# Optimization experiments

Hardware: AMD Instinct MI355X
Metric: run time of the kernel (lower is better)

## Reference

```python
import jax, jax.numpy as jnp
import numpy as np

N_NODES = 100000
N_EDGES = 1600000
N_GRAPHS = 2048
HID = 64
IN_F = 14
N_CLS = 2
EPS = 1e-5


def _gcn_conv(x, row, col, w_edge, W, b, n_nodes):
    # PyG GCNConv with add_self_loops=True, normalize=True.
    xw = x @ W  # [N, out]
    # degree on target nodes, self-loop contributes weight 1
    deg = jnp.zeros((n_nodes,), x.dtype).at[col].add(w_edge) + 1.0
    dinv = deg ** -0.5
    norm = dinv[row] * w_edge * dinv[col]  # [E]
    out = jnp.zeros_like(xw).at[col].add(norm[:, None] * xw[row])
    out = out + (dinv * dinv)[:, None] * xw  # self-loop term
    return out + b


def _bn_relu(x, gamma, beta):
    mean = jnp.mean(x, axis=0)
    var = jnp.var(x, axis=0)  # biased, as PyTorch BN training normalization
    y = gamma * (x - mean) * jax.lax.rsqrt(var + EPS) + beta
    return jax.nn.relu(y)


def setup_inputs() -> dict:
    key = jax.random.key(0)
    ks = jax.random.split(key, 8)
    x = jax.random.normal(ks[0], (N_NODES, IN_F), dtype=jnp.float32)
    edge_index = jax.random.randint(ks[1], (2, N_EDGES), 0, N_NODES, dtype=jnp.int64)
    batch = jnp.sort(jax.random.randint(ks[2], (N_NODES,), 0, N_GRAPHS, dtype=jnp.int64))
    edge_weight = jnp.ones((N_EDGES,), dtype=jnp.float32)
    def lin(k, fi, fo):
        s = 1.0 / np.sqrt(fi)
        kw, kb = jax.random.split(k)
        return (jax.random.uniform(kw, (fi, fo), jnp.float32, -s, s),
                jax.random.uniform(kb, (fo,), jnp.float32, -s, s))
    W1, b1 = lin(ks[3], IN_F, HID)
    W2, b2 = lin(ks[4], HID, HID)
    W3, b3 = lin(ks[5], HID, HID)
    fcW, fcb = lin(ks[6], HID, N_CLS)
    g = jnp.ones((HID,), jnp.float32)
    z = jnp.zeros((HID,), jnp.float32)
    return {
        "x": x, "edge_index": edge_index, "batch": batch, "edge_weight": edge_weight,
        "W1": W1, "b1": b1, "W2": W2, "b2": b2, "W3": W3, "b3": b3,
        "g1": g, "bt1": z, "g2": g, "bt2": z, "g3": g, "bt3": z,
        "fcW": fcW, "fcb": fcb,
    }


def reference(x, edge_index, batch, edge_weight, W1, b1, W2, b2, W3, b3,
              g1, bt1, g2, bt2, g3, bt3, fcW, fcb):
    row, col = edge_index[0], edge_index[1]
    n = x.shape[0]
    h = _bn_relu(_gcn_conv(x, row, col, edge_weight, W1, b1, n), g1, bt1)
    h = _bn_relu(_gcn_conv(h, row, col, edge_weight, W2, b2, n), g2, bt2)
    h = _bn_relu(_gcn_conv(h, row, col, edge_weight, W3, b3, n), g3, bt3)
    node_embs = h  # dropout p=0 is identity
    graph_emb = jax.ops.segment_sum(node_embs, batch, num_segments=N_GRAPHS)
    out = graph_emb @ fcW + fcb
    return (out, node_embs, graph_emb)
```

## Files before the change

### kernel.cpp

```cpp
#include <hip/hip_runtime.h>
#include <hip/hip_fp16.h>

#define N_NODES 100000
#define N_EDGES 1600000
#define EMAX2   2000000
#define N_GRAPHS 2048
#define HID 64
#define IN_F 14
#define N_CLS 2
#define EPS 1e-5f

#define BSHIFT 9
#define NBUCK 196
#define ABLOCKS 256
#define CHUNK (N_EDGES / ABLOCKS)

#define NBLK2 128
#define NCHUNK2 ((N_NODES + NBLK2 - 1) / NBLK2)

typedef _Float16 half_t;
typedef _Float16 half8 __attribute__((ext_vector_type(8)));
typedef float f32x4 __attribute__((ext_vector_type(4)));

#define GSTRIDE ((size_t)N_NODES * 16)


__global__ __launch_bounds__(256) void histA_kernel(const int* __restrict__ col,
                                                    int* __restrict__ histG) {
    __shared__ int hl[NBUCK];
    for (int i = threadIdx.x; i < NBUCK; i += 256) hl[i] = 0;
    __syncthreads();
    int e0 = blockIdx.x * CHUNK;
    for (int e = e0 + threadIdx.x; e < e0 + CHUNK; e += 256)
        atomicAdd(&hl[col[e] >> BSHIFT], 1);
    __syncthreads();
    for (int i = threadIdx.x; i < NBUCK; i += 256)
        histG[i * ABLOCKS + blockIdx.x] = hl[i];
}

__global__ __launch_bounds__(256) void scanS1_kernel(const int* __restrict__ histG,
                                                     int* __restrict__ bsumA) {
    __shared__ int ls[256];
    ls[threadIdx.x] = histG[blockIdx.x * 256 + threadIdx.x];
    __syncthreads();
    for (int off = 128; off > 0; off >>= 1) {
        if (threadIdx.x < off) ls[threadIdx.x] += ls[threadIdx.x + off];
        __syncthreads();
    }
    if (threadIdx.x == 0) bsumA[blockIdx.x] = ls[0];
}

__global__ __launch_bounds__(512) void topscan_kernel(int* __restrict__ bsum, int nb) {
    __shared__ int ls[512];
    int t = threadIdx.x;
    int v = (t < nb) ? bsum[t] : 0;
    ls[t] = v;
    __syncthreads();
    for (int off = 1; off < 512; off <<= 1) {
        int x = ls[t];
        if (t >= off) x += ls[t - off];
        __syncthreads();
        ls[t] = x;
        __syncthreads();
    }
    if (t < nb) bsum[t] = ls[t] - v;
}

__global__ __launch_bounds__(256) void scanS3_kernel(int* __restrict__ histG,
                                                     const int* __restrict__ bsumA,
                                                     int* __restrict__ ptr) {
    __shared__ int ls[256];
    int idx = blockIdx.x * 256 + threadIdx.x;
    int v = histG[idx];
    ls[threadIdx.x] = v;
    __syncthreads();
    for (int off = 1; off < 256; off <<= 1) {
        int x = ls[threadIdx.x];
        if (threadIdx.x >= off) x += ls[threadIdx.x - off];
        __syncthreads();
        ls[threadIdx.x] = x;
        __syncthreads();
    }
    histG[idx] = ls[threadIdx.x] - v + bsumA[blockIdx.x];
    if (blockIdx.x == 0 && threadIdx.x == 0) ptr[N_NODES] = N_EDGES;
}

__global__ __launch_bounds__(256) void scatterA_kernel(const int* __restrict__ row,
                                                       const int* __restrict__ col,
                                                       const float* __restrict__ w,
                                                       const int* __restrict__ histG,
                                                       int2* __restrict__ EA) {
    __shared__ int cur[NBUCK];
    for (int i = threadIdx.x; i < NBUCK; i += 256)
        cur[i] = histG[i * ABLOCKS + blockIdx.x];
    __syncthreads();
    int e0 = blockIdx.x * CHUNK;
    for (int e = e0 + threadIdx.x; e < e0 + CHUNK; e += 256) {
        int c = col[e];
        int r = row[e];
        int fx = (int)__float2uint_rn(w[e] * 8192.0f);
        int pos = atomicAdd(&cur[c >> BSHIFT], 1);
        EA[pos] = make_int2(r, (fx << 17) | c);
    }
}

__global__ __launch_bounds__(256) void bucketA_kernel(const int2* __restrict__ EA,
                                                      const int* __restrict__ bsumA,
                                                      int* __restrict__ ptr,
                                                      float* __restrict__ dinv) {
    __shared__ int hist[512], wsum[512];
    int b = blockIdx.x;
    int beg = bsumA[b];
    int end = (b == NBUCK - 1) ? N_EDGES : bsumA[b + 1];
    int i0 = threadIdx.x, i1 = threadIdx.x + 256;
    hist[i0] = 0; hist[i1] = 0;
    wsum[i0] = 0; wsum[i1] = 0;
    __syncthreads();
    for (int e = beg + threadIdx.x; e < end; e += 256) {
        int2 ed = EA[e];
        int c9 = ed.y & 511;
        atomicAdd(&hist[c9], 1);
        atomicAdd(&wsum[c9], (int)((unsigned int)ed.y >> 17));
    }
    __syncthreads();
    int cnt0 = hist[i0], cnt1 = hist[i1];
    for (int off = 1; off < 512; off <<= 1) {
        int v0 = hist[i0], v1 = hist[i1];
        int a0 = (i0 >= off) ? hist[i0 - off] : 0;
        int a1 = (i1 >= off) ? hist[i1 - off] : 0;
        __syncthreads();
        hist[i0] = v0 + a0;
        hist[i1] = v1 + a1;
        __syncthreads();
    }
    int excl0 = hist[i0] - cnt0, excl1 = hist[i1] - cnt1;
    int col0 = (b << BSHIFT) + i0, col1 = (b << BSHIFT) + i1;
    if (col0 < N_NODES) {
        ptr[col0] = beg + excl0;
        dinv[col0] = rsqrtf(1.0f + (float)wsum[i0] * (1.0f / 8192.0f));
    }
    if (col1 < N_NODES) {
        ptr[col1] = beg + excl1;
        dinv[col1] = rsqrtf(1.0f + (float)wsum[i1] * (1.0f / 8192.0f));
    }
}


__global__ __launch_bounds__(256) void histD_kernel(const int* __restrict__ ptr,
                                                    int* __restrict__ histD) {
    __shared__ int hl[2048];
    for (int i = threadIdx.x; i < 2048; i += 256) hl[i] = 0;
    __syncthreads();
    int n0 = blockIdx.x * NCHUNK2;
    int n1 = n0 + NCHUNK2; if (n1 > N_NODES) n1 = N_NODES;
    for (int n = n0 + threadIdx.x; n < n1; n += 256) {
        int d = ptr[n + 1] - ptr[n];
        if (d > 255) d = 255;
        atomicAdd(&hl[((threadIdx.x & 7) << 8) + d], 1);
    }
    __syncthreads();
    int s = 0;
#pragma unroll
    for (int c = 0; c < 8; c++) s += hl[(c << 8) + threadIdx.x];
    histD[threadIdx.x * NBLK2 + blockIdx.x] = s;
}

__global__ __launch_bounds__(128) void scanD1_kernel(const int* __restrict__ histD,
                                                     int* __restrict__ rowTot) {
    __shared__ int ls[128];
    ls[threadIdx.x] = histD[blockIdx.x * NBLK2 + threadIdx.x];
    __syncthreads();
    for (int off = 64; off > 0; off >>= 1) {
        if (threadIdx.x < off) ls[threadIdx.x] += ls[threadIdx.x + off];
        __syncthreads();
    }
    if (threadIdx.x == 0) rowTot[blockIdx.x] = ls[0];
}

__global__ __launch_bounds__(256) void topscanD_kernel(const int* __restrict__ rowTot,
                                                       int* __restrict__ nodeExcl,
                                                       int* __restrict__ edgeExcl,
                                                       int* __restrict__ ptrS) {
    __shared__ int a[256], b[256];
    int t = threadIdx.x;
    int cnt = rowTot[t];
    int dpad = (t + 3) & ~3;
    int ec = cnt * dpad;
    a[t] = cnt; b[t] = ec;
    __syncthreads();
    for (int off = 1; off < 256; off <<= 1) {
        int va = a[t], vb = b[t];
        if (t >= off) { va += a[t - off]; vb += b[t - off]; }
        __syncthreads();
        a[t] = va; b[t] = vb;
        __syncthreads();
    }
    nodeExcl[t] = a[t] - cnt;
    edgeExcl[t] = b[t] - ec;
    if (t == 255) ptrS[N_NODES] = b[255];
}

__global__ __launch_bounds__(128) void scanD3_kernel(int* __restrict__ histD,
                                                     const int* __restrict__ nodeExcl) {
    __shared__ int ls[128];
    int idx = blockIdx.x * NBLK2 + threadIdx.x;
    int v = histD[idx];
    ls[threadIdx.x] = v;
    __syncthreads();
    for (int off = 1; off < 128; off <<= 1) {
        int x = ls[threadIdx.x];
        if (threadIdx.x >= off) x += ls[threadIdx.x - off];
        __syncthreads();
        ls[threadIdx.x] = x;
        __syncthreads();
    }
    histD[idx] = ls[threadIdx.x] - v + nodeExcl[blockIdx.x];
}

__global__ __launch_bounds__(256) void scatterD_kernel(const int* __restrict__ ptr,
                                                       const int* __restrict__ histD,
                                                       const int* __restrict__ nodeExcl,
                                                       const int* __restrict__ edgeExcl,
                                                       int* __restrict__ perm,
                                                       int* __restrict__ ptrS,
                                                       int* __restrict__ newbase) {
    __shared__ int cur[256];
    cur[threadIdx.x] = histD[threadIdx.x * NBLK2 + blockIdx.x];
    __syncthreads();
    int n0 = blockIdx.x * NCHUNK2;
    int n1 = n0 + NCHUNK2; if (n1 > N_NODES) n1 = N_NODES;
    for (int n = n0 + threadIdx.x; n < n1; n += 256) {
        int d = ptr[n + 1] - ptr[n];
        if (d > 255) d = 255;
        int dpad = (d + 3) & ~3;
        int pos = atomicAdd(&cur[d], 1);
        int ebase = edgeExcl[d] + (pos - nodeExcl[d]) * dpad;
        perm[pos] = n;
        ptrS[pos] = ebase;
        newbase[n] = ebase;
    }
}

__global__ __launch_bounds__(256) void bucketB_kernel(const int2* __restrict__ EA,
                                                      const int* __restrict__ bsumA,
                                                      const int* __restrict__ newbase,
                                                      const float* __restrict__ dinv,
                                                      unsigned int* __restrict__ srcoff,
                                                      half_t* __restrict__ normh) {
    __shared__ int cur[512];
    int b = blockIdx.x;
    int beg = bsumA[b];
    int end = (b == NBUCK - 1) ? N_EDGES : bsumA[b + 1];
    int i0 = threadIdx.x, i1 = threadIdx.x + 256;
    int col0 = (b << BSHIFT) + i0, col1 = (b << BSHIFT) + i1;
    cur[i0] = (col0 < N_NODES) ? newbase[col0] : 0;
    cur[i1] = (col1 < N_NODES) ? newbase[col1] : 0;
    __syncthreads();
    for (int e = beg + threadIdx.x; e < end; e += 256) {
        int2 ed = EA[e];
        int c = ed.y & 0x1ffff;
        float w = (float)((unsigned int)ed.y >> 17) * (1.0f / 8192.0f);
        float nrm = dinv[ed.x] * w * dinv[c];
        int pos = atomicAdd(&cur[c & 511], 1);
        srcoff[pos] = (unsigned int)ed.x << 5;
        normh[pos] = (half_t)nrm;
    }
}


template <int K>
__global__ __launch_bounds__(256) void gemm_kernel(const float* __restrict__ h,
                                                   const float* __restrict__ W,
                                                   half_t* __restrict__ xw, int n_nodes) {
    int f = threadIdx.x & 63;
    float wcol[K];
#pragma unroll
    for (int k = 0; k < K; k++) wcol[k] = W[k * HID + f];
    half_t* xg = xw + (size_t)(f >> 4) * GSTRIDE + (f & 15);
    int wave = (blockIdx.x * blockDim.x + threadIdx.x) >> 6;
    int nwaves = (gridDim.x * blockDim.x) >> 6;
    for (int n = wave; n < n_nodes; n += nwaves) {
        const float* hr = h + (size_t)n * K;
        float acc = 0.f;
#pragma unroll
        for (int k = 0; k < K; k++) acc += hr[k] * wcol[k];
        xg[(size_t)n * 16] = (half_t)acc;
    }
}

__global__ __launch_bounds__(256) void gemm_bn_mfma_kernel(const half_t* __restrict__ h,
                                                           const float* __restrict__ W,
                                                           const float* __restrict__ stats,
                                                           const float* __restrict__ gamma,
                                                           const float* __restrict__ beta,
                                                           half_t* __restrict__ xw, int n_nodes) {
    __shared__ float sc_s[HID], sh_s[HID];
    if (threadIdx.x < 64) {
        float mean = stats[threadIdx.x] * (1.0f / N_NODES);
        float var = stats[64 + threadIdx.x] * (1.0f / N_NODES) - mean * mean;
        float sc = gamma[threadIdx.x] * rsqrtf(var + EPS);
        sc_s[threadIdx.x] = sc;
        sh_s[threadIdx.x] = beta[threadIdx.x] - mean * sc;
    }
    __syncthreads();
    int lane = threadIdx.x & 63;
    int col16 = lane & 15;
    int quad = lane >> 4;

    float scA[2][8], shA[2][8];
#pragma unroll
    for (int kh = 0; kh < 2; kh++)
#pragma unroll
        for (int j = 0; j < 8; j++) {
            int k = kh * 32 + quad * 8 + j;
            scA[kh][j] = sc_s[k];
            shA[kh][j] = sh_s[k];
        }

    half8 bfrag[4][2];
#pragma unroll
    for (int t = 0; t < 4; t++)
#pragma unroll
        for (int kh = 0; kh < 2; kh++)
#pragma unroll
            for (int j = 0; j < 8; j++) {
                int k = kh * 32 + quad * 8 + j;
                bfrag[t][kh][j] = (half_t)W[k * HID + t * 16 + col16];
            }

    int wave = (blockIdx.x * blockDim.x + threadIdx.x) >> 6;
    int nwaves = (gridDim.x * blockDim.x) >> 6;
    int ntiles = n_nodes >> 4;
    for (int tIdx = wave; tIdx < ntiles; tIdx += nwaves) {
        int n0 = tIdx << 4;
        half8 afrag[2];
#pragma unroll
        for (int kh = 0; kh < 2; kh++) {
            int k0 = kh * 32 + quad * 8;
            const half_t* hp = h + (size_t)(k0 >> 4) * GSTRIDE
                                 + (size_t)(n0 + col16) * 16 + (k0 & 15);
            half8 raw = *(const half8*)hp;
#pragma unroll
            for (int j = 0; j < 8; j++) {
                float v = (float)raw[j] * scA[kh][j] + shA[kh][j];
                afrag[kh][j] = (half_t)fmaxf(v, 0.f);
            }
        }
        f32x4 acc[4];
#pragma unroll
        for (int t = 0; t < 4; t++) {
            f32x4 z = {0.f, 0.f, 0.f, 0.f};
            acc[t] = __builtin_amdgcn_mfma_f32_16x16x32_f16(afrag[0], bfrag[t][0], z, 0, 0, 0);
            acc[t] = __builtin_amdgcn_mfma_f32_16x16x32_f16(afrag[1], bfrag[t][1], acc[t], 0, 0, 0);
        }
#pragma unroll
        for (int t = 0; t < 4; t++) {
            half_t* xg = xw + (size_t)t * GSTRIDE;
#pragma unroll
            for (int r = 0; r < 4; r++) {
                int rowi = n0 + quad * 4 + r;
                xg[(size_t)rowi * 16 + col16] = (half_t)acc[t][r];
            }
        }
    }
}

__global__ __launch_bounds__(256) void gather_stats_kernel(const int* __restrict__ ptrS,
                                                           const int* __restrict__ perm,
                                                           const unsigned int* __restrict__ srcoff,
                                                           const unsigned int* __restrict__ normu,
                                                           const half_t* __restrict__ xw,
                                                           const float* __restrict__ dinv,
                                                           const float* __restrict__ b,
                                                           half_t* __restrict__ hp,
                                                           float* __restrict__ stats,
                                                           int n_nodes) {
    int g = (blockIdx.x & 7) >> 1;
    int grank = ((blockIdx.x >> 3) << 1) | (blockIdx.x & 1);
    int lane16 = threadIdx.x & 15;
    int quadLocal = threadIdx.x >> 4;
    int quadId = grank * 16 + quadLocal;
    int nquads = (gridDim.x >> 2) * 16;

    const half_t* xg = xw + (size_t)g * GSTRIDE;
    const char* xgc = (const char*)xg;
    unsigned int loff = (unsigned int)(lane16 * 2);
    half_t* hpg = hp + (size_t)g * GSTRIDE;
    int f = g * 16 + lane16;
    float bf = b[f];
    int base = ((threadIdx.x & 63) >> 4) * 16;

    float s = 0.f, s2 = 0.f;

    int npairs = n_nodes >> 1;
    int idx = quadId;
    int nodeA = 0, begA = 0, cA = 0, nodeB = 0, begB = 0, cB = 0;
    int evA = 0, nvA = 0, evB = 0, nvB = 0;
    if (idx < npairs) {
        int iA = idx * 2;
        nodeA = perm[iA];
        nodeB = perm[iA + 1];
        begA = ptrS[iA];
        begB = ptrS[iA + 1];
        cA = begB - begA;
        cB = ptrS[iA + 2] - begB;
        int mA = (cA > 16) ? 16 : cA;
        int mB = (cB > 16) ? 16 : cB;
        if (lane16 < mA) evA = (int)srcoff[begA + lane16];
        if (lane16 < (mA >> 1)) nvA = (int)normu[(begA >> 1) + lane16];
        if (lane16 < mB) evB = (int)srcoff[begB + lane16];
        if (lane16 < (mB >> 1)) nvB = (int)normu[(begB >> 1) + lane16];
    }

    while (idx < npairs) {
        int inext = idx + nquads;
        int nodeA2 = 0, begA2 = 0, cA2 = 0, nodeB2 = 0, begB2 = 0, cB2 = 0;
        if (inext < npairs) {
            int iN = inext * 2;
            nodeA2 = perm[iN];
            nodeB2 = perm[iN + 1];
            begA2 = ptrS[iN];
            begB2 = ptrS[iN + 1];
            cA2 = begB2 - begA2;
            cB2 = ptrS[iN + 2] - begB2;
        }
        float selfA = (float)xg[(size_t)nodeA * 16 + lane16];
        float diA = dinv[nodeA];
        float selfB = (float)xg[(size_t)nodeB * 16 + lane16];
        float diB = dinv[nodeB];

        __half2 aA0 = __float2half2_rn(0.f), aA1 = __float2half2_rn(0.f);
        __half2 aB0 = __float2half2_rn(0.f), aB1 = __float2half2_rn(0.f);

        for (int j0 = 0; j0 < cB; j0 += 16) {
            int mA = cA - j0; mA = (mA < 0) ? 0 : ((mA > 16) ? 16 : mA);
            int mB = cB - j0; mB = (mB > 16) ? 16 : mB;
            int pA = mA >> 1;
            int pB = mB >> 1;
            int evA2 = 0, nvA2 = 0, evB2 = 0, nvB2 = 0;
            int j1 = j0 + 16;
            if (j1 < cA) {
                int m2 = cA - j1; if (m2 > 16) m2 = 16;
                if (lane16 < m2) evA2 = (int)srcoff[begA + j1 + lane16];
                if (lane16 < (m2 >> 1)) nvA2 = (int)normu[((begA + j1) >> 1) + lane16];
            }
            if (j1 < cB) {
                int m2 = cB - j1; if (m2 > 16) m2 = 16;
                if (lane16 < m2) evB2 = (int)srcoff[begB + j1 + lane16];
                if (lane16 < (m2 >> 1)) nvB2 = (int)normu[((begB + j1) >> 1) + lane16];
            }
            for (int p = 0; p < pB; p += 2) {
                unsigned int ub0 = (unsigned int)__shfl(evB, base + 2 * p);
                unsigned int ub1 = (unsigned int)__shfl(evB, base + 2 * p + 1);
                unsigned int ub2 = (unsigned int)__shfl(evB, base + 2 * p + 2);
                unsigned int ub3 = (unsigned int)__shfl(evB, base + 2 * p + 3);
                unsigned int nb0 = (unsigned int)__shfl(nvB, base + p);
                unsigned int nb1 = (unsigned int)__shfl(nvB, base + p + 1);
                __half hb0 = *(const __half*)(xgc + (ub0 + loff));
                __half hb1 = *(const __half*)(xgc + (ub1 + loff));
                __half hb2 = *(const __half*)(xgc + (ub2 + loff));
                __half hb3 = *(const __half*)(xgc + (ub3 + loff));
                aB0 = __hfma2(*(__half2*)&nb0, __halves2half2(hb0, hb1), aB0);
                aB1 = __hfma2(*(__half2*)&nb1, __halves2half2(hb2, hb3), aB1);
                if (p < pA) {
                    unsigned int ua0 = (unsigned int)__shfl(evA, base + 2 * p);
                    unsigned int ua1 = (unsigned int)__shfl(evA, base + 2 * p + 1);
                    unsigned int ua2 = (unsigned int)__shfl(evA, base + 2 * p + 2);
                    unsigned int ua3 = (unsigned int)__shfl(evA, base + 2 * p + 3);
                    unsigned int na0 = (unsigned int)__shfl(nvA, base + p);
                    unsigned int na1 = (unsigned int)__shfl(nvA, base + p + 1);
                    __half ha0 = *(const __half*)(xgc + (ua0 + loff));
                    __half ha1 = *(const __half*)(xgc + (ua1 + loff));
                    __half ha2 = *(const __half*)(xgc + (ua2 + loff));
                    __half ha3 = *(const __half*)(xgc + (ua3 + loff));
                    aA0 = __hfma2(*(__half2*)&na0, __halves2half2(ha0, ha1), aA0);
                    aA1 = __hfma2(*(__half2*)&na1, __halves2half2(ha2, ha3), aA1);
                }
            }
            evA = evA2; nvA = nvA2; evB = evB2; nvB = nvB2;
        }
        if (inext < npairs) {
            int mA0 = (cA2 > 16) ? 16 : cA2;
            int mB0 = (cB2 > 16) ? 16 : cB2;
            evA = (lane16 < mA0) ? (int)srcoff[begA2 + lane16] : 0;
            nvA = (lane16 < (mA0 >> 1)) ? (int)normu[(begA2 >> 1) + lane16] : 0;
            evB = (lane16 < mB0) ? (int)srcoff[begB2 + lane16] : 0;
            nvB = (lane16 < (mB0 >> 1)) ? (int)normu[(begB2 >> 1) + lane16] : 0;
        }

        float accA = (__low2float(aA0) + __high2float(aA0))
                   + (__low2float(aA1) + __high2float(aA1));
        float vA = accA + diA * diA * selfA + bf;
        hpg[(size_t)nodeA * 16 + lane16] = (half_t)vA;
        float accB = (__low2float(aB0) + __high2float(aB0))
                   + (__low2float(aB1) + __high2float(aB1));
        float vB = accB + diB * diB * selfB + bf;
        hpg[(size_t)nodeB * 16 + lane16] = (half_t)vB;
        s += vA + vB;
        s2 += vA * vA + vB * vB;

        idx = inext;
        nodeA = nodeA2; begA = begA2; cA = cA2;
        nodeB = nodeB2; begB = begB2; cB = cB2;
    }
    __shared__ float ls[256], ls2[256];
    ls[threadIdx.x] = s;
    ls2[threadIdx.x] = s2;
    __syncthreads();
    if (threadIdx.x < 16) {
        float a = 0.f, aa = 0.f;
#pragma unroll
        for (int k = 0; k < 16; k++) {
            a += ls[k * 16 + threadIdx.x];
            aa += ls2[k * 16 + threadIdx.x];
        }
        atomicAdd(&stats[g * 16 + threadIdx.x], a);
        atomicAdd(&stats[64 + g * 16 + threadIdx.x], aa);
    }
}

__global__ __launch_bounds__(256) void bn_relu_seg_kernel(const half_t* __restrict__ hpl,
                                                          float* __restrict__ h3,
                                                          const float* __restrict__ stats,
                                                          const float* __restrict__ gamma,
                                                          const float* __restrict__ beta,
                                                          const int* __restrict__ batch,
                                                          float* __restrict__ gemb,
                                                          int n_nodes) {
    int g = blockIdx.x * blockDim.x + threadIdx.x;
    int f = g & 63;
    int wave = g >> 6;
    int nwaves = (gridDim.x * blockDim.x) >> 6;
    int chunk = (n_nodes + nwaves - 1) / nwaves;
    int n0 = wave * chunk;
    int n1 = n0 + chunk;
    if (n1 > n_nodes) n1 = n_nodes;
    if (n0 >= n_nodes) return;
    float mean = stats[f] * (1.0f / N_NODES);
    float var = stats[64 + f] * (1.0f / N_NODES) - mean * mean;
    float sc = gamma[f] * rsqrtf(var + EPS);
    float sh = beta[f] - mean * sc;
    const half_t* hg = hpl + (size_t)(f >> 4) * GSTRIDE + (f & 15);
    int curg = batch[n0];
    float racc = 0.f;
    for (int n = n0; n < n1; n++) {
        int bg = batch[n];
        if (bg != curg) {
            atomicAdd(&gemb[(size_t)curg * HID + f], racc);
            racc = 0.f;
            curg = bg;
        }
        float v = (float)hg[(size_t)n * 16] * sc + sh;
        v = fmaxf(v, 0.f);
        h3[(size_t)n * HID + f] = v;
        racc += v;
    }
    atomicAdd(&gemb[(size_t)curg * HID + f], racc);
}

__global__ __launch_bounds__(256) void final_kernel(const float* __restrict__ gemb,
                                                    const float* __restrict__ fcW,
                                                    const float* __restrict__ fcb,
                                                    float* __restrict__ out) {
    int g = blockIdx.x * blockDim.x + threadIdx.x;
    if (g >= N_GRAPHS * N_CLS) return;
    int gr = g >> 1, c = g & 1;
    float acc = fcb[c];
#pragma unroll
    for (int k = 0; k < HID; k++) acc += gemb[gr * HID + k] * fcW[k * N_CLS + c];
    out[g] = acc;
}


extern "C" void kernel_launch(void* const* d_in, const int* in_sizes, int n_in,
                              void* d_out, int out_size, void* d_ws, size_t ws_size,
                              hipStream_t stream) {
    const float* x    = (const float*)d_in[0];
    const int*   ei   = (const int*)d_in[1];
    const int*   batch= (const int*)d_in[2];
    const float* ew   = (const float*)d_in[3];
    const float* W1   = (const float*)d_in[4];
    const float* b1   = (const float*)d_in[5];
    const float* W2   = (const float*)d_in[6];
    const float* b2   = (const float*)d_in[7];
    const float* W3   = (const float*)d_in[8];
    const float* b3   = (const float*)d_in[9];
    const float* g1   = (const float*)d_in[10];
    const float* bt1  = (const float*)d_in[11];
    const float* g2   = (const float*)d_in[12];
    const float* bt2  = (const float*)d_in[13];
    const float* g3   = (const float*)d_in[14];
    const float* bt3  = (const float*)d_in[15];
    const float* fcW  = (const float*)d_in[16];
    const float* fcb  = (const float*)d_in[17];

    const int* row = ei;
    const int* col = ei + N_EDGES;

    float* out_head  = (float*)d_out;
    float* node_embs = out_head + N_GRAPHS * N_CLS;
    float* gemb      = node_embs + (size_t)N_NODES * HID;

    char* bse = (char*)d_ws;
    half_t* xwh = (half_t*)bse;
    char* r1 = bse + (size_t)N_NODES * HID * 2;
    int2*   EA  = (int2*)r1;
    half_t* hpl = (half_t*)r1;
    char* r2 = r1 + (size_t)N_NODES * HID * 2;
    unsigned int* srcoff = (unsigned int*)r2;
    half_t* normh = (half_t*)(srcoff + EMAX2);
    char* r3 = r2 + (size_t)EMAX2 * 6;
    float* dinv  = (float*)r3;
    float* stats3 = dinv + N_NODES;
    int*   ptr   = (int*)(stats3 + 384);
    int*   histG = ptr + N_NODES + 1;
    int*   bsumA = histG + NBUCK * ABLOCKS;
    int*   histD = bsumA + NBUCK + 4;
    int*   rowTot = histD + 256 * NBLK2;
    int*   nodeExcl = rowTot + 256;
    int*   edgeExcl = nodeExcl + 256;
    int*   perm   = edgeExcl + 256;
    int*   newbase= perm + N_NODES;
    int*   ptrS   = newbase + N_NODES;

    const int B   = 256;
    const int gGS = 1024;
    const int gGA = 2048;

    hipMemsetAsync(srcoff, 0, (size_t)EMAX2 * 6, stream);
    hipMemsetAsync(stats3, 0, 384 * sizeof(float), stream);
    hipMemsetAsync(gemb, 0, (size_t)N_GRAPHS * HID * sizeof(float), stream);

    histA_kernel<<<ABLOCKS, B, 0, stream>>>(col, histG);
    scanS1_kernel<<<NBUCK, B, 0, stream>>>(histG, bsumA);
    topscan_kernel<<<1, 512, 0, stream>>>(bsumA, NBUCK);
    scanS3_kernel<<<NBUCK, B, 0, stream>>>(histG, bsumA, ptr);
    scatterA_kernel<<<ABLOCKS, B, 0, stream>>>(row, col, ew, histG, EA);
    bucketA_kernel<<<NBUCK, B, 0, stream>>>(EA, bsumA, ptr, dinv);

    histD_kernel<<<NBLK2, B, 0, stream>>>(ptr, histD);
    scanD1_kernel<<<256, 128, 0, stream>>>(histD, rowTot);
    topscanD_kernel<<<1, 256, 0, stream>>>(rowTot, nodeExcl, edgeExcl, ptrS);
    scanD3_kernel<<<256, 128, 0, stream>>>(histD, nodeExcl);
    scatterD_kernel<<<NBLK2, B, 0, stream>>>(ptr, histD, nodeExcl, edgeExcl,
                                             perm, ptrS, newbase);
    bucketB_kernel<<<NBUCK, B, 0, stream>>>(EA, bsumA, newbase, dinv, srcoff, normh);

    float* h3 = node_embs;

    gemm_kernel<IN_F><<<gGS, B, 0, stream>>>(x, W1, xwh, N_NODES);
    gather_stats_kernel<<<gGA, B, 0, stream>>>(ptrS, perm, srcoff,
                                               (const unsigned int*)normh, xwh,
                                               dinv, b1, hpl, stats3, N_NODES);

    gemm_bn_mfma_kernel<<<gGS, B, 0, stream>>>(hpl, W2, stats3, g1, bt1, xwh, N_NODES);
    gather_stats_kernel<<<gGA, B, 0, stream>>>(ptrS, perm, srcoff,
                                               (const unsigned int*)normh, xwh,
                                               dinv, b2, hpl, stats3 + 128, N_NODES);

    gemm_bn_mfma_kernel<<<gGS, B, 0, stream>>>(hpl, W3, stats3 + 128, g2, bt2, xwh, N_NODES);
    gather_stats_kernel<<<gGA, B, 0, stream>>>(ptrS, perm, srcoff,
                                               (const unsigned int*)normh, xwh,
                                               dinv, b3, hpl, stats3 + 256, N_NODES);

    bn_relu_seg_kernel<<<gGS, B, 0, stream>>>(hpl, h3, stats3 + 256, g3, bt3,
                                              batch, gemb, N_NODES);

    final_kernel<<<(N_GRAPHS * N_CLS + B - 1) / B, B, 0, stream>>>(gemb, fcW, fcb, out_head);
}
```

Before: 414.7 us.

## Fold dinv scaling into GEMM output, balance gather work, fuse scans and memsets

The symmetric normalization is restructured so the GEMM outputs are pre-scaled by dinv[src] and the gather applies dinv[dst] once, which lets the edge stream carry raw weights instead of per-edge norms. A new qbounds kernel binary-searches the padded edge prefix so each quad gets a contiguous, roughly equal-work range of nodes instead of a strided slice. The top-level scan kernels are folded into the per-block scan kernels. The large memsets are replaced by zeroing only the padding slots and by clearing gemb and stats inside histA. This removes several launches and a large memset, and trims per-edge gather loads, at the cost of redundant scan work in every block and reliance on the padding being zeroed so the gather can read full 16-lane groups unconditionally.

```diff
diff --git a/kernel.cpp b/kernel.cpp
--- a/kernel.cpp
+++ b/kernel.cpp
@@ -18,6 +18,8 @@
 #define NBLK2 128
 #define NCHUNK2 ((N_NODES + NBLK2 - 1) / NBLK2)
 
+#define NQUADS 8192
+
 typedef _Float16 half_t;
 typedef _Float16 half8 __attribute__((ext_vector_type(8)));
 typedef float f32x4 __attribute__((ext_vector_type(4)));
@@ -26,9 +28,14 @@
 
 
 __global__ __launch_bounds__(256) void histA_kernel(const int* __restrict__ col,
-                                                    int* __restrict__ histG) {
+                                                    int* __restrict__ histG,
+                                                    float* __restrict__ gemb,
+                                                    float* __restrict__ stats3) {
     __shared__ int hl[NBUCK];
     for (int i = threadIdx.x; i < NBUCK; i += 256) hl[i] = 0;
+    for (int k = threadIdx.x; k < 512; k += 256)
+        gemb[(size_t)blockIdx.x * 512 + k] = 0.f;
+    if (blockIdx.x == 0 && threadIdx.x < 384) stats3[threadIdx.x] = 0.f;
     __syncthreads();
     int e0 = blockIdx.x * CHUNK;
     for (int e = e0 + threadIdx.x; e < e0 + CHUNK; e += 256)
@@ -50,39 +57,30 @@
     if (threadIdx.x == 0) bsumA[blockIdx.x] = ls[0];
 }
 
-__global__ __launch_bounds__(512) void topscan_kernel(int* __restrict__ bsum, int nb) {
-    __shared__ int ls[512];
-    int t = threadIdx.x;
-    int v = (t < nb) ? bsum[t] : 0;
-    ls[t] = v;
-    __syncthreads();
-    for (int off = 1; off < 512; off <<= 1) {
-        int x = ls[t];
-        if (t >= off) x += ls[t - off];
-        __syncthreads();
-        ls[t] = x;
-        __syncthreads();
-    }
-    if (t < nb) bsum[t] = ls[t] - v;
-}
-
 __global__ __launch_bounds__(256) void scanS3_kernel(int* __restrict__ histG,
                                                      const int* __restrict__ bsumA,
+                                                     int* __restrict__ bsumX,
                                                      int* __restrict__ ptr) {
-    __shared__ int ls[256];
-    int idx = blockIdx.x * 256 + threadIdx.x;
+    __shared__ int ls[256], bs[256];
+    int t = threadIdx.x;
+    int rawB = (blockIdx.x < NBUCK) ? bsumA[blockIdx.x] : 0;
+    bs[t] = (t < NBUCK) ? bsumA[t] : 0;
+    int idx = blockIdx.x * 256 + t;
     int v = histG[idx];
-    ls[threadIdx.x] = v;
+    ls[t] = v;
     __syncthreads();
     for (int off = 1; off < 256; off <<= 1) {
-        int x = ls[threadIdx.x];
-        if (threadIdx.x >= off) x += ls[threadIdx.x - off];
-        __syncthreads();
-        ls[threadIdx.x] = x;
-        __syncthreads();
-    }
-    histG[idx] = ls[threadIdx.x] - v + bsumA[blockIdx.x];
-    if (blockIdx.x == 0 && threadIdx.x == 0) ptr[N_NODES] = N_EDGES;
+        int x = ls[t];
+        int y = bs[t];
+        if (t >= off) { x += ls[t - off]; y += bs[t - off]; }
+        __syncthreads();
+        ls[t] = x; bs[t] = y;
+        __syncthreads();
+    }
+    int bexcl = bs[blockIdx.x] - rawB;
+    histG[idx] = ls[t] - v + bexcl;
+    if (t == 0) bsumX[blockIdx.x] = bexcl;
+    if (blockIdx.x == 0 && t == 0) ptr[N_NODES] = N_EDGES;
 }
 
 __global__ __launch_bounds__(256) void scatterA_kernel(const int* __restrict__ row,
@@ -105,13 +103,13 @@
 }
 
 __global__ __launch_bounds__(256) void bucketA_kernel(const int2* __restrict__ EA,
-                                                      const int* __restrict__ bsumA,
+                                                      const int* __restrict__ bsumX,
                                                       int* __restrict__ ptr,
                                                       float* __restrict__ dinv) {
     __shared__ int hist[512], wsum[512];
     int b = blockIdx.x;
-    int beg = bsumA[b];
-    int end = (b == NBUCK - 1) ? N_EDGES : bsumA[b + 1];
+    int beg = bsumX[b];
+    int end = (b == NBUCK - 1) ? N_EDGES : bsumX[b + 1];
     int i0 = threadIdx.x, i1 = threadIdx.x + 256;
     hist[i0] = 0; hist[i1] = 0;
     wsum[i0] = 0; wsum[i1] = 0;
@@ -177,44 +175,50 @@
     if (threadIdx.x == 0) rowTot[blockIdx.x] = ls[0];
 }
 
-__global__ __launch_bounds__(256) void topscanD_kernel(const int* __restrict__ rowTot,
-                                                       int* __restrict__ nodeExcl,
-                                                       int* __restrict__ edgeExcl,
-                                                       int* __restrict__ ptrS) {
-    __shared__ int a[256], b[256];
+__global__ __launch_bounds__(128) void scanD3_kernel(int* __restrict__ histD,
+                                                     const int* __restrict__ rowTot,
+                                                     int* __restrict__ nodeExcl,
+                                                     int* __restrict__ edgeExcl,
+                                                     int* __restrict__ ptrS) {
+    __shared__ int ls[128], sa[256], sb[256];
     int t = threadIdx.x;
-    int cnt = rowTot[t];
-    int dpad = (t + 3) & ~3;
-    int ec = cnt * dpad;
-    a[t] = cnt; b[t] = ec;
+    int bin = blockIdx.x;
+    int c0 = rowTot[t], c1 = rowTot[t + 128];
+    sa[t] = c0;           sa[t + 128] = c1;
+    sb[t] = c0 * ((t + 3) & ~3);
+    sb[t + 128] = c1 * ((t + 131) & ~3);
+    int idx = bin * NBLK2 + t;
+    int v = histD[idx];
+    ls[t] = v;
     __syncthreads();
     for (int off = 1; off < 256; off <<= 1) {
-        int va = a[t], vb = b[t];
-        if (t >= off) { va += a[t - off]; vb += b[t - off]; }
-        __syncthreads();
-        a[t] = va; b[t] = vb;
-        __syncthreads();
-    }
-    nodeExcl[t] = a[t] - cnt;
-    edgeExcl[t] = b[t] - ec;
-    if (t == 255) ptrS[N_NODES] = b[255];
-}
-
-__global__ __launch_bounds__(128) void scanD3_kernel(int* __restrict__ histD,
-                                                     const int* __restrict__ nodeExcl) {
-    __shared__ int ls[128];
-    int idx = blockIdx.x * NBLK2 + threadIdx.x;
-    int v = histD[idx];
-    ls[threadIdx.x] = v;
-    __syncthreads();
+        int a0 = sa[t], a1 = sa[t + 128];
+        int b0 = sb[t], b1 = sb[t + 128];
+        int x0 = (t >= off) ? sa[t - off] : 0;
+        int x1 = (t + 128 >= off) ? sa[t + 128 - off] : 0;
+        int y0 = (t >= off) ? sb[t - off] : 0;
+        int y1 = (t + 128 >= off) ? sb[t + 128 - off] : 0;
+        __syncthreads();
+        sa[t] = a0 + x0; sa[t + 128] = a1 + x1;
+        sb[t] = b0 + y0; sb[t + 128] = b1 + y1;
+        __syncthreads();
+    }
     for (int off = 1; off < 128; off <<= 1) {
-        int x = ls[threadIdx.x];
-        if (threadIdx.x >= off) x += ls[threadIdx.x - off];
-        __syncthreads();
-        ls[threadIdx.x] = x;
-        __syncthreads();
-    }
-    histD[idx] = ls[threadIdx.x] - v + nodeExcl[blockIdx.x];
+        int x = ls[t];
+        if (t >= off) x += ls[t - off];
+        __syncthreads();
+        ls[t] = x;
+        __syncthreads();
+    }
+    int nE = sa[bin] - rowTot[bin];
+    histD[idx] = ls[t] - v + nE;
+    if (bin == 0) {
+        nodeExcl[t] = sa[t] - rowTot[t];
+        nodeExcl[t + 128] = sa[t + 128] - rowTot[t + 128];
+        edgeExcl[t] = sb[t] - rowTot[t] * ((t + 3) & ~3);
+        edgeExcl[t + 128] = sb[t + 128] - rowTot[t + 128] * ((t + 131) & ~3);
+        if (t == 127) ptrS[N_NODES] = sb[255];
+    }
 }
 
 __global__ __launch_bounds__(256) void scatterD_kernel(const int* __restrict__ ptr,
@@ -223,7 +227,9 @@
                                                        const int* __restrict__ edgeExcl,
                                                        int* __restrict__ perm,
                                                        int* __restrict__ ptrS,
-                                                       int* __restrict__ newbase) {
+                                                       int* __restrict__ newbase,
+                                                       unsigned int* __restrict__ srcoff,
+                                                       half_t* __restrict__ normh) {
     __shared__ int cur[256];
     cur[threadIdx.x] = histD[threadIdx.x * NBLK2 + blockIdx.x];
     __syncthreads();
@@ -238,19 +244,38 @@
         perm[pos] = n;
         ptrS[pos] = ebase;
         newbase[n] = ebase;
-    }
+        for (int k = d; k < dpad; k++) {
+            srcoff[ebase + k] = 0u;
+            normh[ebase + k] = (half_t)0.f;
+        }
+    }
+}
+
+__global__ __launch_bounds__(256) void qbounds_kernel(const int* __restrict__ ptrS,
+                                                      int* __restrict__ qlo) {
+    int q = blockIdx.x * 256 + threadIdx.x;
+    if (q > NQUADS) return;
+    if (q == NQUADS) { qlo[q] = N_NODES; return; }
+    long long W = (long long)ptrS[N_NODES] + 8LL * N_NODES;
+    long long target = (W * q) / NQUADS;
+    int lo = 0, hi = N_NODES;
+    while (lo < hi) {
+        int mid = (lo + hi) >> 1;
+        long long f = (long long)ptrS[mid] + 8LL * mid;
+        if (f < target) lo = mid + 1; else hi = mid;
+    }
+    qlo[q] = lo & ~1;
 }
 
 __global__ __launch_bounds__(256) void bucketB_kernel(const int2* __restrict__ EA,
-                                                      const int* __restrict__ bsumA,
+                                                      const int* __restrict__ bsumX,
                                                       const int* __restrict__ newbase,
-                                                      const float* __restrict__ dinv,
                                                       unsigned int* __restrict__ srcoff,
                                                       half_t* __restrict__ normh) {
     __shared__ int cur[512];
     int b = blockIdx.x;
-    int beg = bsumA[b];
-    int end = (b == NBUCK - 1) ? N_EDGES : bsumA[b + 1];
+    int beg = bsumX[b];
+    int end = (b == NBUCK - 1) ? N_EDGES : bsumX[b + 1];
     int i0 = threadIdx.x, i1 = threadIdx.x + 256;
     int col0 = (b << BSHIFT) + i0, col1 = (b << BSHIFT) + i1;
     cur[i0] = (col0 < N_NODES) ? newbase[col0] : 0;
@@ -260,10 +285,9 @@
         int2 ed = EA[e];
         int c = ed.y & 0x1ffff;
         float w = (float)((unsigned int)ed.y >> 17) * (1.0f / 8192.0f);
-        float nrm = dinv[ed.x] * w * dinv[c];
         int pos = atomicAdd(&cur[c & 511], 1);
         srcoff[pos] = (unsigned int)ed.x << 5;
-        normh[pos] = (half_t)nrm;
+        normh[pos] = (half_t)w;
     }
 }
 
@@ -271,6 +295,7 @@
 template <int K>
 __global__ __launch_bounds__(256) void gemm_kernel(const float* __restrict__ h,
                                                    const float* __restrict__ W,
+                                                   const float* __restrict__ dinv,
                                                    half_t* __restrict__ xw, int n_nodes) {
     int f = threadIdx.x & 63;
     float wcol[K];
@@ -284,7 +309,7 @@
         float acc = 0.f;
 #pragma unroll
         for (int k = 0; k < K; k++) acc += hr[k] * wcol[k];
-        xg[(size_t)n * 16] = (half_t)acc;
+        xg[(size_t)n * 16] = (half_t)(acc * dinv[n]);
     }
 }
 
@@ -293,6 +318,7 @@
                                                            const float* __restrict__ stats,
                                                            const float* __restrict__ gamma,
                                                            const float* __restrict__ beta,
+                                                           const float* __restrict__ dinv,
                                                            half_t* __restrict__ xw, int n_nodes) {
     __shared__ float sc_s[HID], sh_s[HID];
     if (threadIdx.x < 64) {
@@ -353,13 +379,14 @@
             acc[t] = __builtin_amdgcn_mfma_f32_16x16x32_f16(afrag[0], bfrag[t][0], z, 0, 0, 0);
             acc[t] = __builtin_amdgcn_mfma_f32_16x16x32_f16(afrag[1], bfrag[t][1], acc[t], 0, 0, 0);
         }
+        f32x4 dv = *(const f32x4*)(dinv + n0 + quad * 4);
 #pragma unroll
         for (int t = 0; t < 4; t++) {
             half_t* xg = xw + (size_t)t * GSTRIDE;
 #pragma unroll
             for (int r = 0; r < 4; r++) {
                 int rowi = n0 + quad * 4 + r;
-                xg[(size_t)rowi * 16 + col16] = (half_t)acc[t][r];
+                xg[(size_t)rowi * 16 + col16] = (half_t)(acc[t][r] * dv[r]);
             }
         }
     }
@@ -374,55 +401,51 @@
                                                            const float* __restrict__ b,
                                                            half_t* __restrict__ hp,
                                                            float* __restrict__ stats,
+                                                           const int* __restrict__ qlo,
                                                            int n_nodes) {
     int g = (blockIdx.x & 7) >> 1;
     int grank = ((blockIdx.x >> 3) << 1) | (blockIdx.x & 1);
     int lane16 = threadIdx.x & 15;
     int quadLocal = threadIdx.x >> 4;
     int quadId = grank * 16 + quadLocal;
-    int nquads = (gridDim.x >> 2) * 16;
 
     const half_t* xg = xw + (size_t)g * GSTRIDE;
     const char* xgc = (const char*)xg;
     unsigned int loff = (unsigned int)(lane16 * 2);
     half_t* hpg = hp + (size_t)g * GSTRIDE;
-    int f = g * 16 + lane16;
-    float bf = b[f];
+    float bf = b[g * 16 + lane16];
     int base = ((threadIdx.x & 63) >> 4) * 16;
 
     float s = 0.f, s2 = 0.f;
 
-    int npairs = n_nodes >> 1;
-    int idx = quadId;
+    int lo = qlo[quadId], hi = qlo[quadId + 1];
+
+    int i = lo;
     int nodeA = 0, begA = 0, cA = 0, nodeB = 0, begB = 0, cB = 0;
     int evA = 0, nvA = 0, evB = 0, nvB = 0;
-    if (idx < npairs) {
-        int iA = idx * 2;
-        nodeA = perm[iA];
-        nodeB = perm[iA + 1];
-        begA = ptrS[iA];
-        begB = ptrS[iA + 1];
+    if (i < hi) {
+        nodeA = perm[i];
+        nodeB = perm[i + 1];
+        begA = ptrS[i];
+        begB = ptrS[i + 1];
         cA = begB - begA;
-        cB = ptrS[iA + 2] - begB;
-        int mA = (cA > 16) ? 16 : cA;
-        int mB = (cB > 16) ? 16 : cB;
-        if (lane16 < mA) evA = (int)srcoff[begA + lane16];
-        if (lane16 < (mA >> 1)) nvA = (int)normu[(begA >> 1) + lane16];
-        if (lane16 < mB) evB = (int)srcoff[begB + lane16];
-        if (lane16 < (mB >> 1)) nvB = (int)normu[(begB >> 1) + lane16];
-    }
-
-    while (idx < npairs) {
-        int inext = idx + nquads;
+        cB = ptrS[i + 2] - begB;
+        evA = (int)srcoff[begA + lane16];
+        nvA = (int)normu[(begA >> 1) + lane16];
+        evB = (int)srcoff[begB + lane16];
+        nvB = (int)normu[(begB >> 1) + lane16];
+    }
+
+    while (i < hi) {
+        int inext = i + 2;
         int nodeA2 = 0, begA2 = 0, cA2 = 0, nodeB2 = 0, begB2 = 0, cB2 = 0;
-        if (inext < npairs) {
-            int iN = inext * 2;
-            nodeA2 = perm[iN];
-            nodeB2 = perm[iN + 1];
-            begA2 = ptrS[iN];
-            begB2 = ptrS[iN + 1];
+        if (inext < hi) {
+            nodeA2 = perm[inext];
+            nodeB2 = perm[inext + 1];
+            begA2 = ptrS[inext];
+            begB2 = ptrS[inext + 1];
             cA2 = begB2 - begA2;
-            cB2 = ptrS[iN + 2] - begB2;
+            cB2 = ptrS[inext + 2] - begB2;
         }
         float selfA = (float)xg[(size_t)nodeA * 16 + lane16];
         float diA = dinv[nodeA];
@@ -440,14 +463,12 @@
             int evA2 = 0, nvA2 = 0, evB2 = 0, nvB2 = 0;
             int j1 = j0 + 16;
             if (j1 < cA) {
-                int m2 = cA - j1; if (m2 > 16) m2 = 16;
-                if (lane16 < m2) evA2 = (int)srcoff[begA + j1 + lane16];
-                if (lane16 < (m2 >> 1)) nvA2 = (int)normu[((begA + j1) >> 1) + lane16];
+                evA2 = (int)srcoff[begA + j1 + lane16];
+                nvA2 = (int)normu[((begA + j1) >> 1) + lane16];
             }
             if (j1 < cB) {
-                int m2 = cB - j1; if (m2 > 16) m2 = 16;
-                if (lane16 < m2) evB2 = (int)srcoff[begB + j1 + lane16];
-                if (lane16 < (m2 >> 1)) nvB2 = (int)normu[((begB + j1) >> 1) + lane16];
+                evB2 = (int)srcoff[begB + j1 + lane16];
+                nvB2 = (int)normu[((begB + j1) >> 1) + lane16];
             }
             for (int p = 0; p < pB; p += 2) {
                 unsigned int ub0 = (unsigned int)__shfl(evB, base + 2 * p);
@@ -479,27 +500,25 @@
             }
             evA = evA2; nvA = nvA2; evB = evB2; nvB = nvB2;
         }
-        if (inext < npairs) {
-            int mA0 = (cA2 > 16) ? 16 : cA2;
-            int mB0 = (cB2 > 16) ? 16 : cB2;
-            evA = (lane16 < mA0) ? (int)srcoff[begA2 + lane16] : 0;
-            nvA = (lane16 < (mA0 >> 1)) ? (int)normu[(begA2 >> 1) + lane16] : 0;
-            evB = (lane16 < mB0) ? (int)srcoff[begB2 + lane16] : 0;
-            nvB = (lane16 < (mB0 >> 1)) ? (int)normu[(begB2 >> 1) + lane16] : 0;
+        if (inext < hi) {
+            evA = (int)srcoff[begA2 + lane16];
+            nvA = (int)normu[(begA2 >> 1) + lane16];
+            evB = (int)srcoff[begB2 + lane16];
+            nvB = (int)normu[(begB2 >> 1) + lane16];
         }
 
         float accA = (__low2float(aA0) + __high2float(aA0))
                    + (__low2float(aA1) + __high2float(aA1));
-        float vA = accA + diA * diA * selfA + bf;
+        float vA = diA * (accA + selfA) + bf;
         hpg[(size_t)nodeA * 16 + lane16] = (half_t)vA;
         float accB = (__low2float(aB0) + __high2float(aB0))
                    + (__low2float(aB1) + __high2float(aB1));
-        float vB = accB + diB * diB * selfB + bf;
+        float vB = diB * (accB + selfB) + bf;
         hpg[(size_t)nodeB * 16 + lane16] = (half_t)vB;
         s += vA + vB;
         s2 += vA * vA + vB * vB;
 
-        idx = inext;
+        i = inext;
         nodeA = nodeA2; begA = begA2; cA = cA2;
         nodeB = nodeB2; begB = begB2; cB = cB2;
     }
@@ -615,53 +634,50 @@
     int*   ptr   = (int*)(stats3 + 384);
     int*   histG = ptr + N_NODES + 1;
     int*   bsumA = histG + NBUCK * ABLOCKS;
-    int*   histD = bsumA + NBUCK + 4;
+    int*   bsumX = bsumA + NBUCK + 4;
+    int*   histD = bsumX + NBUCK + 4;
     int*   rowTot = histD + 256 * NBLK2;
     int*   nodeExcl = rowTot + 256;
     int*   edgeExcl = nodeExcl + 256;
     int*   perm   = edgeExcl + 256;
     int*   newbase= perm + N_NODES;
     int*   ptrS   = newbase + N_NODES;
+    int*   qlo    = ptrS + N_NODES + 1;
 
     const int B   = 256;
     const int gGS = 1024;
     const int gGA = 2048;
 
-    hipMemsetAsync(srcoff, 0, (size_t)EMAX2 * 6, stream);
-    hipMemsetAsync(stats3, 0, 384 * sizeof(float), stream);
-    hipMemsetAsync(gemb, 0, (size_t)N_GRAPHS * HID * sizeof(float), stream);
-
-    histA_kernel<<<ABLOCKS, B, 0, stream>>>(col, histG);
+    histA_kernel<<<ABLOCKS, B, 0, stream>>>(col, histG, gemb, stats3);
     scanS1_kernel<<<NBUCK, B, 0, stream>>>(histG, bsumA);
-    topscan_kernel<<<1, 512, 0, stream>>>(bsumA, NBUCK);
-    scanS3_kernel<<<NBUCK, B, 0, stream>>>(histG, bsumA, ptr);
+    scanS3_kernel<<<NBUCK, B, 0, stream>>>(histG, bsumA, bsumX, ptr);
     scatterA_kernel<<<ABLOCKS, B, 0, stream>>>(row, col, ew, histG, EA);
-    bucketA_kernel<<<NBUCK, B, 0, stream>>>(EA, bsumA, ptr, dinv);
+    bucketA_kernel<<<NBUCK, B, 0, stream>>>(EA, bsumX, ptr, dinv);
 
     histD_kernel<<<NBLK2, B, 0, stream>>>(ptr, histD);
     scanD1_kernel<<<256, 128, 0, stream>>>(histD, rowTot);
-    topscanD_kernel<<<1, 256, 0, stream>>>(rowTot, nodeExcl, edgeExcl, ptrS);
-    scanD3_kernel<<<256, 128, 0, stream>>>(histD, nodeExcl);
+    scanD3_kernel<<<256, 128, 0, stream>>>(histD, rowTot, nodeExcl, edgeExcl, ptrS);
     scatterD_kernel<<<NBLK2, B, 0, stream>>>(ptr, histD, nodeExcl, edgeExcl,
-                                             perm, ptrS, newbase);
-    bucketB_kernel<<<NBUCK, B, 0, stream>>>(EA, bsumA, newbase, dinv, srcoff, normh);
+                                             perm, ptrS, newbase, srcoff, normh);
+    qbounds_kernel<<<(NQUADS + 256) / 256, B, 0, stream>>>(ptrS, qlo);
+    bucketB_kernel<<<NBUCK, B, 0, stream>>>(EA, bsumX, newbase, srcoff, normh);
 
     float* h3 = node_embs;
 
-    gemm_kernel<IN_F><<<gGS, B, 0, stream>>>(x, W1, xwh, N_NODES);
+    gemm_kernel<IN_F><<<gGS, B, 0, stream>>>(x, W1, dinv, xwh, N_NODES);
     gather_stats_kernel<<<gGA, B, 0, stream>>>(ptrS, perm, srcoff,
                                                (const unsigned int*)normh, xwh,
-                                               dinv, b1, hpl, stats3, N_NODES);
-
-    gemm_bn_mfma_kernel<<<gGS, B, 0, stream>>>(hpl, W2, stats3, g1, bt1, xwh, N_NODES);
+                                               dinv, b1, hpl, stats3, qlo, N_NODES);
+
+    gemm_bn_mfma_kernel<<<gGS, B, 0, stream>>>(hpl, W2, stats3, g1, bt1, dinv, xwh, N_NODES);
     gather_stats_kernel<<<gGA, B, 0, stream>>>(ptrS, perm, srcoff,
                                                (const unsigned int*)normh, xwh,
-                                               dinv, b2, hpl, stats3 + 128, N_NODES);
-
-    gemm_bn_mfma_kernel<<<gGS, B, 0, stream>>>(hpl, W3, stats3 + 128, g2, bt2, xwh, N_NODES);
+                                               dinv, b2, hpl, stats3 + 128, qlo, N_NODES);
+
+    gemm_bn_mfma_kernel<<<gGS, B, 0, stream>>>(hpl, W3, stats3 + 128, g2, bt2, dinv, xwh, N_NODES);
     gather_stats_kernel<<<gGA, B, 0, stream>>>(ptrS, perm, srcoff,
                                                (const unsigned int*)normh, xwh,
-                                               dinv, b3, hpl, stats3 + 256, N_NODES);
+                                               dinv, b3, hpl, stats3 + 256, qlo, N_NODES);
 
     bn_relu_seg_kernel<<<gGS, B, 0, stream>>>(hpl, h3, stats3 + 256, g3, bt3,
                                               batch, gemb, N_NODES);
```

Result: slower. 455.7 us (+9.9%).
